# Performance work log

Hardware: AMD Instinct MI355X
Metric: run time of the kernel (lower is better)

Reference implementation:

```python
import jax, jax.numpy as jnp
import numpy as np

N, E = 100000, 1600000
IN, H, C, OUT = 128, 4, 32, 64  # in_channels, heads, hidden_channels, out_channels


def setup_inputs() -> dict:
    key = jax.random.key(0)
    ks = jax.random.split(key, 9)
    x = jax.random.normal(ks[0], (N, IN), dtype=jnp.float32)
    edge_index = jax.random.randint(ks[1], (2, E), 0, N, dtype=jnp.int64)
    s = 1.0 / np.sqrt(IN)
    W = jax.random.uniform(ks[2], (IN, H * C), jnp.float32, -s, s)
    att_src = jax.random.uniform(ks[3], (H, C), jnp.float32, -s, s)
    att_dst = jax.random.uniform(ks[4], (H, C), jnp.float32, -s, s)
    bias = jnp.zeros((H * C,), jnp.float32)
    sl = 1.0 / np.sqrt(H * C)
    lin_w = jax.random.uniform(ks[5], (H * C, OUT), jnp.float32, -sl, sl)
    lin_b = jax.random.uniform(ks[6], (OUT,), jnp.float32, -sl, sl)
    return {"x": x, "edge_index": edge_index, "W": W, "att_src": att_src,
            "att_dst": att_dst, "bias": bias, "lin_w": lin_w, "lin_b": lin_b}


def reference(x, edge_index, W, att_src, att_dst, bias, lin_w, lin_b):
    n = x.shape[0]
    # PyG GATConv default: add self-loops
    loops = jnp.arange(n, dtype=edge_index.dtype)
    src = jnp.concatenate([edge_index[0], loops])  # message sources
    dst = jnp.concatenate([edge_index[1], loops])  # message targets
    h = (x @ W).reshape(n, H, C)                   # [N,H,C]
    a_src = (h * att_src).sum(-1)                  # [N,H]
    a_dst = (h * att_dst).sum(-1)                  # [N,H]
    e = jax.nn.leaky_relu(a_src[src] + a_dst[dst], 0.2)  # [E',H]
    # segment softmax over incoming edges per destination node
    m = jax.ops.segment_max(e, dst, num_segments=n)
    m = jnp.where(jnp.isfinite(m), m, 0.0)
    ex = jnp.exp(e - m[dst])
    denom = jax.ops.segment_sum(ex, dst, num_segments=n)
    alpha = ex / (denom[dst] + 1e-16)              # [E',H]
    agg = jax.ops.segment_sum(h[src] * alpha[:, :, None], dst, num_segments=n)  # [N,H,C]
    out = agg.reshape(n, H * C) + bias
    out = jax.nn.relu(out)  # dropout is identity in eval mode
    return out @ lin_w + lin_b
```

## Files before the change

### kernel.cpp

```cpp
#include <hip/hip_runtime.h>
#include <math.h>

#define NND 100000
#define NED 1600000

#define CAP 64

#define NRANGE 8
#define RNG_NODES ((NND + NRANGE - 1) / NRANGE)
#define NCHUNK 640
#define CHUNK_E (NED / NCHUNK)

#define GEMM_NB (NND / 32)
#define GROUPS 640
#define GRID_NB (GROUPS * 13)

#define OFF_HB    ((size_t)0)
#define OFF_YS    ((size_t)25600000)
#define OFF_ASRC  ((size_t)51200000)
#define OFF_ADST  ((size_t)52800000)
#define OFF_SRT   ((size_t)54400000)
#define OFF_WF    ((size_t)80000000)
#define OFF_CUR   ((size_t)80049152)

typedef __attribute__((ext_vector_type(8))) short short8;
typedef __attribute__((ext_vector_type(4))) float f32x4;

__device__ __forceinline__ float leaky02(float v) { return v > 0.f ? v : 0.2f * v; }

__device__ __forceinline__ unsigned short f2bf(float f) {
    unsigned u = __float_as_uint(f);
    return (unsigned short)((u + 0x7fffu + ((u >> 16) & 1u)) >> 16);
}

__global__ __launch_bounds__(256)
void k_wprep(const float* __restrict__ W, const float* __restrict__ lin_w,
             unsigned short* __restrict__ wf, int* __restrict__ cur) {
    const int idx = blockIdx.x * 256 + threadIdx.x;
    if (blockIdx.x >= 12) {
        const int i = (blockIdx.x - 12) * 256 + threadIdx.x;
        if (i < NND) cur[i] = 0;
        return;
    }
    if (idx < 2048) {
        const int l  = idx & 63;
        const int ks = (idx >> 6) & 3;
        const int ct = (idx >> 8) & 1;
        const int wv = idx >> 9;
        const int col = wv * 32 + ct * 16 + (l & 15);
        const int k0  = ks * 32 + (l >> 4) * 8;
#pragma unroll
        for (int j = 0; j < 8; ++j)
            wf[idx * 8 + j] = f2bf(W[(size_t)(k0 + j) * 128 + col]);
    } else if (idx < 3072) {
        const int i2 = idx - 2048;
        const int l  = i2 & 63;
        const int ks = (i2 >> 6) & 3;
        const int wv = i2 >> 8;
        const int col = wv * 16 + (l & 15);
        const int k0  = ks * 32 + (l >> 4) * 8;
#pragma unroll
        for (int j = 0; j < 8; ++j)
            wf[idx * 8 + j] = f2bf(lin_w[(size_t)(k0 + j) * 64 + col]);
    }
}

__global__ __launch_bounds__(256)
void k_front(const int* __restrict__ esrc, const int* __restrict__ edst,
             int* __restrict__ cur, int* __restrict__ ssrt,
             const float* __restrict__ x, const unsigned short* __restrict__ wf,
             const float* __restrict__ att_s, const float* __restrict__ att_d,
             unsigned short* __restrict__ hb,
             float* __restrict__ a_src, float* __restrict__ a_dst)
{
    __shared__ unsigned short xb[32 * 128];

    const int g = blockIdx.x / 13;
    const int r13 = blockIdx.x % 13;

    if (r13 < 8) {
        const int dlo = r13 * RNG_NODES;
        const int dhi = min(NND, dlo + RNG_NODES);
        const int elo = g * CHUNK_E;
        const int ehi = elo + CHUNK_E;

        int e = elo + threadIdx.x;
        for (; e + 768 < ehi; e += 1024) {
            const int d0 = edst[e];
            const int d1 = edst[e + 256];
            const int d2 = edst[e + 512];
            const int d3 = edst[e + 768];
            const int s0 = esrc[e];
            const int s1 = esrc[e + 256];
            const int s2 = esrc[e + 512];
            const int s3 = esrc[e + 768];
            if (d0 >= dlo && d0 < dhi) { const int p = atomicAdd(&cur[d0], 1); if (p < CAP - 1) ssrt[d0 * CAP + 1 + p] = s0; }
            if (d1 >= dlo && d1 < dhi) { const int p = atomicAdd(&cur[d1], 1); if (p < CAP - 1) ssrt[d1 * CAP + 1 + p] = s1; }
            if (d2 >= dlo && d2 < dhi) { const int p = atomicAdd(&cur[d2], 1); if (p < CAP - 1) ssrt[d2 * CAP + 1 + p] = s2; }
            if (d3 >= dlo && d3 < dhi) { const int p = atomicAdd(&cur[d3], 1); if (p < CAP - 1) ssrt[d3 * CAP + 1 + p] = s3; }
        }
        for (; e < ehi; e += 256) {
            const int d = edst[e];
            if (d >= dlo && d < dhi) {
                const int p = atomicAdd(&cur[d], 1);
                if (p < CAP - 1) ssrt[d * CAP + 1 + p] = esrc[e];
            }
        }
        return;
    }

    const int gb = g * 5 + (r13 - 8);
    if (gb >= GEMM_NB) return;
    const int tid = threadIdx.x;
    const int wv = tid >> 6;
    const int l = tid & 63;
    const int lg = l >> 4;
    const int lc = l & 15;
    const int row0 = gb * 32;

    const float4* x4 = (const float4*)(x + (size_t)row0 * 128);
#pragma unroll
    for (int i = 0; i < 4; ++i) {
        const int g2 = tid + 256 * i;
        const int row = g2 >> 5;
        const int kq = g2 & 31;
        const float4 v = x4[g2];
        uint2 p;
        p.x = (unsigned)f2bf(v.x) | ((unsigned)f2bf(v.y) << 16);
        p.y = (unsigned)f2bf(v.z) | ((unsigned)f2bf(v.w) << 16);
        const int byteoff = (row * 256 + kq * 8) ^ ((row & 7) << 4);
        *(uint2*)((char*)xb + byteoff) = p;
    }

    short8 bf[2][4];
#pragma unroll
    for (int ct = 0; ct < 2; ++ct)
#pragma unroll
        for (int ks = 0; ks < 4; ++ks)
            bf[ct][ks] = *(const short8*)(wf + (size_t)((((wv * 2 + ct) * 4 + ks) * 64 + l) * 8));

    __syncthreads();

    f32x4 acc[2][2];
#pragma unroll
    for (int rt = 0; rt < 2; ++rt)
#pragma unroll
        for (int ct = 0; ct < 2; ++ct)
            acc[rt][ct] = (f32x4){0.f, 0.f, 0.f, 0.f};

#pragma unroll
    for (int ks = 0; ks < 4; ++ks) {
        short8 a[2];
#pragma unroll
        for (int rt = 0; rt < 2; ++rt) {
            const int row = rt * 16 + lc;
            const int byteoff = (row * 256 + (ks * 32 + lg * 8) * 2) ^ ((row & 7) << 4);
            a[rt] = *(const short8*)((const char*)xb + byteoff);
        }
#pragma unroll
        for (int rt = 0; rt < 2; ++rt)
#pragma unroll
            for (int ct = 0; ct < 2; ++ct)
                acc[rt][ct] = __builtin_amdgcn_mfma_f32_16x16x32_bf16(
                    a[rt], bf[ct][ks], acc[rt][ct], 0, 0, 0);
    }

    const int c0 = wv * 32 + lc;
    const float as0 = att_s[c0], as1 = att_s[c0 + 16];
    const float ad0 = att_d[c0], ad1 = att_d[c0 + 16];

#pragma unroll
    for (int rt = 0; rt < 2; ++rt) {
#pragma unroll
        for (int r = 0; r < 4; ++r) {
            const int row = row0 + rt * 16 + lg * 4 + r;
            const float h0 = acc[rt][0][r];
            const float h1 = acc[rt][1][r];
            hb[(size_t)row * 128 + c0]      = f2bf(h0);
            hb[(size_t)row * 128 + c0 + 16] = f2bf(h1);
            float vs = h0 * as0 + h1 * as1;
            float vd = h0 * ad0 + h1 * ad1;
#pragma unroll
            for (int o = 8; o > 0; o >>= 1) {
                vs += __shfl_xor(vs, o, 64);
                vd += __shfl_xor(vd, o, 64);
            }
            if (lc == 0) {
                a_src[row * 4 + wv] = vs;
                a_dst[row * 4 + wv] = vd;
            }
        }
    }
}

__global__ __launch_bounds__(256)
void k_fused(const int* __restrict__ cur, const int* __restrict__ ssrt,
             const float* __restrict__ a_src, const float* __restrict__ a_dst,
             const unsigned short* __restrict__ hb, const float* __restrict__ bias,
             unsigned short* __restrict__ ysb)
{
    __shared__ int   s_src[4][64];
    __shared__ float s_alp[4][64][4];
    const int lane = threadIdx.x & 63;
    const int wv = threadIdx.x >> 6;
    const int d = blockIdx.x * 4 + wv;
    if (d >= NND) return;
    const int cnt = min(cur[d], CAP - 1) + 1;
    const float4 ad = *(const float4*)(a_dst + (size_t)d * 4);

    int s = d;
    float4 ex = make_float4(0.f, 0.f, 0.f, 0.f);
    if (lane < cnt) {
        s = (lane == 0) ? d : ssrt[d * CAP + lane];
        const float4 as = *(const float4*)(a_src + (size_t)s * 4);
        ex.x = __expf(leaky02(as.x + ad.x));
        ex.y = __expf(leaky02(as.y + ad.y));
        ex.z = __expf(leaky02(as.z + ad.z));
        ex.w = __expf(leaky02(as.w + ad.w));
    }
    float4 sm = ex;
#pragma unroll
    for (int o = 32; o > 0; o >>= 1) {
        sm.x += __shfl_xor(sm.x, o, 64);
        sm.y += __shfl_xor(sm.y, o, 64);
        sm.z += __shfl_xor(sm.z, o, 64);
        sm.w += __shfl_xor(sm.w, o, 64);
    }
    const float4 iv = make_float4(1.f / (sm.x + 1e-16f), 1.f / (sm.y + 1e-16f),
                                  1.f / (sm.z + 1e-16f), 1.f / (sm.w + 1e-16f));
    if (lane < cnt) {
        s_src[wv][lane] = s;
        const float4 al = make_float4(ex.x * iv.x, ex.y * iv.y,
                                      ex.z * iv.z, ex.w * iv.w);
        *(float4*)&s_alp[wv][lane][0] = al;
    }

    const int hsel = lane >> 4;
    float accx = 0.f, accy = 0.f;
    int k = 0;
    for (; k + 8 <= cnt; k += 8) {
        int sv[8];
        float Av[8];
        unsigned uv[8];
#pragma unroll
        for (int q = 0; q < 8; ++q) {
            sv[q] = __builtin_amdgcn_readfirstlane(s_src[wv][k + q]);
            Av[q] = s_alp[wv][k + q][hsel];
        }
#pragma unroll
        for (int q = 0; q < 8; ++q)
            uv[q] = *(const unsigned*)(hb + (size_t)sv[q] * 128 + 2 * lane);
#pragma unroll
        for (int q = 0; q < 8; ++q) {
            accx += __uint_as_float(uv[q] << 16) * Av[q];
            accy += __uint_as_float(uv[q] & 0xffff0000u) * Av[q];
        }
    }
    for (; k < cnt; ++k) {
        const int s2 = __builtin_amdgcn_readfirstlane(s_src[wv][k]);
        const float A = s_alp[wv][k][hsel];
        const unsigned u = *(const unsigned*)(hb + (size_t)s2 * 128 + 2 * lane);
        accx += __uint_as_float(u << 16) * A;
        accy += __uint_as_float(u & 0xffff0000u) * A;
    }
    const float2 bb = *(const float2*)(bias + 2 * lane);
    float ox = accx + bb.x, oy = accy + bb.y;
    ox = ox > 0.f ? ox : 0.f;
    oy = oy > 0.f ? oy : 0.f;
    const unsigned up = (unsigned)f2bf(ox) | ((unsigned)f2bf(oy) << 16);
    *(unsigned*)(ysb + (size_t)d * 128 + 2 * lane) = up;
}

__global__ __launch_bounds__(256)
void k_out(const unsigned short* __restrict__ ysb, const unsigned short* __restrict__ wf,
           const float* __restrict__ lin_b, float* __restrict__ out)
{
    __shared__ unsigned short yb[32 * 128];
    const int tid = threadIdx.x;
    const int wv = tid >> 6;
    const int l = tid & 63;
    const int lg = l >> 4;
    const int lc = l & 15;
    const int row0 = blockIdx.x * 32;

    const uint2* ysrc = (const uint2*)(ysb + (size_t)row0 * 128);
#pragma unroll
    for (int i = 0; i < 4; ++i) {
        const int g = tid + 256 * i;
        const int row = g >> 5;
        const int kq = g & 31;
        const uint2 v = ysrc[g];
        const int byteoff = (row * 256 + kq * 8) ^ ((row & 7) << 4);
        *(uint2*)((char*)yb + byteoff) = v;
    }

    short8 bf[4];
#pragma unroll
    for (int ks = 0; ks < 4; ++ks)
        bf[ks] = *(const short8*)(wf + (size_t)((2048 + (wv * 4 + ks) * 64 + l) * 8));

    __syncthreads();

    f32x4 acc[2];
    acc[0] = (f32x4){0.f, 0.f, 0.f, 0.f};
    acc[1] = (f32x4){0.f, 0.f, 0.f, 0.f};

#pragma unroll
    for (int ks = 0; ks < 4; ++ks) {
        short8 a[2];
#pragma unroll
        for (int rt = 0; rt < 2; ++rt) {
            const int row = rt * 16 + lc;
            const int byteoff = (row * 256 + (ks * 32 + lg * 8) * 2) ^ ((row & 7) << 4);
            a[rt] = *(const short8*)((const char*)yb + byteoff);
        }
#pragma unroll
        for (int rt = 0; rt < 2; ++rt)
            acc[rt] = __builtin_amdgcn_mfma_f32_16x16x32_bf16(a[rt], bf[ks], acc[rt], 0, 0, 0);
    }

    const int col = wv * 16 + lc;
    const float lb = lin_b[col];
#pragma unroll
    for (int rt = 0; rt < 2; ++rt) {
#pragma unroll
        for (int r = 0; r < 4; ++r) {
            const int row = row0 + rt * 16 + lg * 4 + r;
            out[(size_t)row * 64 + col] = acc[rt][r] + lb;
        }
    }
}

extern "C" void kernel_launch(void* const* d_in, const int* in_sizes, int n_in,
                              void* d_out, int out_size, void* d_ws, size_t ws_size,
                              hipStream_t stream)
{
    const float* x     = (const float*)d_in[0];
    const int*   ei    = (const int*)  d_in[1];
    const float* W     = (const float*)d_in[2];
    const float* att_s = (const float*)d_in[3];
    const float* att_d = (const float*)d_in[4];
    const float* bias  = (const float*)d_in[5];
    const float* lin_w = (const float*)d_in[6];
    const float* lin_b = (const float*)d_in[7];
    float* out = (float*)d_out;

    const int* esrc = ei;
    const int* edst = ei + NED;

    char* ws = (char*)d_ws;
    unsigned short* hb  = (unsigned short*)(ws + OFF_HB);
    unsigned short* ysb = (unsigned short*)(ws + OFF_YS);
    float* a_src = (float*)(ws + OFF_ASRC);
    float* a_dst = (float*)(ws + OFF_ADST);
    int*   ssrt  = (int*)  (ws + OFF_SRT);
    unsigned short* wf = (unsigned short*)(ws + OFF_WF);
    int*   cur  = (int*)  (ws + OFF_CUR);

    k_wprep<<<12 + (NND + 255) / 256, 256, 0, stream>>>(W, lin_w, wf, cur);

    k_front<<<GRID_NB, 256, 0, stream>>>(esrc, edst, cur, ssrt,
                                         x, wf, att_s, att_d,
                                         hb, a_src, a_dst);

    k_fused<<<(NND + 3) / 4, 256, 0, stream>>>(cur, ssrt, a_src, a_dst,
                                               hb, bias, ysb);

    k_out<<<NND / 32, 256, 0, stream>>>(ysb, wf, lin_b, out);
}
```

Baseline: 172.2 us.

## Fuse attention aggregation with output linear into a single back kernel

Merges the per-destination softmax/aggregation kernel and the output projection MFMA kernel into one kernel. Each block handles 32 destination rows, with each wave processing 8 rows serially, writing the bf16 activations straight into swizzled shared memory and then running the MFMA projection. This removes the global ysb round-trip (write plus reread, about 25 MB) and one kernel launch. In exchange, each wave now covers 8 rows in sequence, so there are fewer independent waves in flight to hide gather latency.

```diff
diff --git a/kernel.cpp b/kernel.cpp
--- a/kernel.cpp
+++ b/kernel.cpp
@@ -16,12 +16,11 @@
 #define GRID_NB (GROUPS * 13)
 
 #define OFF_HB    ((size_t)0)
-#define OFF_YS    ((size_t)25600000)
-#define OFF_ASRC  ((size_t)51200000)
-#define OFF_ADST  ((size_t)52800000)
-#define OFF_SRT   ((size_t)54400000)
-#define OFF_WF    ((size_t)80000000)
-#define OFF_CUR   ((size_t)80049152)
+#define OFF_ASRC  ((size_t)25600000)
+#define OFF_ADST  ((size_t)27200000)
+#define OFF_SRT   ((size_t)28800000)
+#define OFF_WF    ((size_t)54400000)
+#define OFF_CUR   ((size_t)54449152)
 
 typedef __attribute__((ext_vector_type(8))) short short8;
 typedef __attribute__((ext_vector_type(4))) float f32x4;
@@ -194,112 +193,101 @@
 }
 
 __global__ __launch_bounds__(256)
-void k_fused(const int* __restrict__ cur, const int* __restrict__ ssrt,
-             const float* __restrict__ a_src, const float* __restrict__ a_dst,
-             const unsigned short* __restrict__ hb, const float* __restrict__ bias,
-             unsigned short* __restrict__ ysb)
+void k_back(const int* __restrict__ cur, const int* __restrict__ ssrt,
+            const float* __restrict__ a_src, const float* __restrict__ a_dst,
+            const unsigned short* __restrict__ hb, const float* __restrict__ bias,
+            const unsigned short* __restrict__ wf, const float* __restrict__ lin_b,
+            float* __restrict__ out)
 {
+    __shared__ unsigned short yb[32 * 128];
     __shared__ int   s_src[4][64];
     __shared__ float s_alp[4][64][4];
-    const int lane = threadIdx.x & 63;
-    const int wv = threadIdx.x >> 6;
-    const int d = blockIdx.x * 4 + wv;
-    if (d >= NND) return;
-    const int cnt = min(cur[d], CAP - 1) + 1;
-    const float4 ad = *(const float4*)(a_dst + (size_t)d * 4);
-
-    int s = d;
-    float4 ex = make_float4(0.f, 0.f, 0.f, 0.f);
-    if (lane < cnt) {
-        s = (lane == 0) ? d : ssrt[d * CAP + lane];
-        const float4 as = *(const float4*)(a_src + (size_t)s * 4);
-        ex.x = __expf(leaky02(as.x + ad.x));
-        ex.y = __expf(leaky02(as.y + ad.y));
-        ex.z = __expf(leaky02(as.z + ad.z));
-        ex.w = __expf(leaky02(as.w + ad.w));
-    }
-    float4 sm = ex;
-#pragma unroll
-    for (int o = 32; o > 0; o >>= 1) {
-        sm.x += __shfl_xor(sm.x, o, 64);
-        sm.y += __shfl_xor(sm.y, o, 64);
-        sm.z += __shfl_xor(sm.z, o, 64);
-        sm.w += __shfl_xor(sm.w, o, 64);
-    }
-    const float4 iv = make_float4(1.f / (sm.x + 1e-16f), 1.f / (sm.y + 1e-16f),
-                                  1.f / (sm.z + 1e-16f), 1.f / (sm.w + 1e-16f));
-    if (lane < cnt) {
-        s_src[wv][lane] = s;
-        const float4 al = make_float4(ex.x * iv.x, ex.y * iv.y,
-                                      ex.z * iv.z, ex.w * iv.w);
-        *(float4*)&s_alp[wv][lane][0] = al;
-    }
-
+    const int tid = threadIdx.x;
+    const int lane = tid & 63;
+    const int wv = tid >> 6;
+    const int base = blockIdx.x * 32;
+
+    const float2 bb = *(const float2*)(bias + 2 * lane);
     const int hsel = lane >> 4;
-    float accx = 0.f, accy = 0.f;
-    int k = 0;
-    for (; k + 8 <= cnt; k += 8) {
-        int sv[8];
-        float Av[8];
-        unsigned uv[8];
-#pragma unroll
-        for (int q = 0; q < 8; ++q) {
-            sv[q] = __builtin_amdgcn_readfirstlane(s_src[wv][k + q]);
-            Av[q] = s_alp[wv][k + q][hsel];
-        }
-#pragma unroll
-        for (int q = 0; q < 8; ++q)
-            uv[q] = *(const unsigned*)(hb + (size_t)sv[q] * 128 + 2 * lane);
-#pragma unroll
-        for (int q = 0; q < 8; ++q) {
-            accx += __uint_as_float(uv[q] << 16) * Av[q];
-            accy += __uint_as_float(uv[q] & 0xffff0000u) * Av[q];
-        }
-    }
-    for (; k < cnt; ++k) {
-        const int s2 = __builtin_amdgcn_readfirstlane(s_src[wv][k]);
-        const float A = s_alp[wv][k][hsel];
-        const unsigned u = *(const unsigned*)(hb + (size_t)s2 * 128 + 2 * lane);
-        accx += __uint_as_float(u << 16) * A;
-        accy += __uint_as_float(u & 0xffff0000u) * A;
-    }
-    const float2 bb = *(const float2*)(bias + 2 * lane);
-    float ox = accx + bb.x, oy = accy + bb.y;
-    ox = ox > 0.f ? ox : 0.f;
-    oy = oy > 0.f ? oy : 0.f;
-    const unsigned up = (unsigned)f2bf(ox) | ((unsigned)f2bf(oy) << 16);
-    *(unsigned*)(ysb + (size_t)d * 128 + 2 * lane) = up;
-}
-
-__global__ __launch_bounds__(256)
-void k_out(const unsigned short* __restrict__ ysb, const unsigned short* __restrict__ wf,
-           const float* __restrict__ lin_b, float* __restrict__ out)
-{
-    __shared__ unsigned short yb[32 * 128];
-    const int tid = threadIdx.x;
-    const int wv = tid >> 6;
-    const int l = tid & 63;
+#pragma unroll 1
+    for (int i = 0; i < 8; ++i) {
+        const int rloc = wv * 8 + i;
+        const int d = base + rloc;
+        const int cnt = min(cur[d], CAP - 1) + 1;
+        const float4 ad = *(const float4*)(a_dst + (size_t)d * 4);
+
+        int s = d;
+        float4 ex = make_float4(0.f, 0.f, 0.f, 0.f);
+        if (lane < cnt) {
+            s = (lane == 0) ? d : ssrt[d * CAP + lane];
+            const float4 as = *(const float4*)(a_src + (size_t)s * 4);
+            ex.x = __expf(leaky02(as.x + ad.x));
+            ex.y = __expf(leaky02(as.y + ad.y));
+            ex.z = __expf(leaky02(as.z + ad.z));
+            ex.w = __expf(leaky02(as.w + ad.w));
+        }
+        float4 sm = ex;
+#pragma unroll
+        for (int o = 32; o > 0; o >>= 1) {
+            sm.x += __shfl_xor(sm.x, o, 64);
+            sm.y += __shfl_xor(sm.y, o, 64);
+            sm.z += __shfl_xor(sm.z, o, 64);
+            sm.w += __shfl_xor(sm.w, o, 64);
+        }
+        const float4 iv = make_float4(1.f / (sm.x + 1e-16f), 1.f / (sm.y + 1e-16f),
+                                      1.f / (sm.z + 1e-16f), 1.f / (sm.w + 1e-16f));
+        if (lane < cnt) {
+            s_src[wv][lane] = s;
+            const float4 al = make_float4(ex.x * iv.x, ex.y * iv.y,
+                                          ex.z * iv.z, ex.w * iv.w);
+            *(float4*)&s_alp[wv][lane][0] = al;
+        }
+
+        float accx = 0.f, accy = 0.f;
+        int k = 0;
+        for (; k + 8 <= cnt; k += 8) {
+            int sv[8];
+            float Av[8];
+            unsigned uv[8];
+#pragma unroll
+            for (int q = 0; q < 8; ++q) {
+                sv[q] = __builtin_amdgcn_readfirstlane(s_src[wv][k + q]);
+                Av[q] = s_alp[wv][k + q][hsel];
+            }
+#pragma unroll
+            for (int q = 0; q < 8; ++q)
+                uv[q] = *(const unsigned*)(hb + (size_t)sv[q] * 128 + 2 * lane);
+#pragma unroll
+            for (int q = 0; q < 8; ++q) {
+                accx += __uint_as_float(uv[q] << 16) * Av[q];
+                accy += __uint_as_float(uv[q] & 0xffff0000u) * Av[q];
+            }
+        }
+        for (; k < cnt; ++k) {
+            const int s2 = __builtin_amdgcn_readfirstlane(s_src[wv][k]);
+            const float A = s_alp[wv][k][hsel];
+            const unsigned u = *(const unsigned*)(hb + (size_t)s2 * 128 + 2 * lane);
+            accx += __uint_as_float(u << 16) * A;
+            accy += __uint_as_float(u & 0xffff0000u) * A;
+        }
+        float ox = accx + bb.x, oy = accy + bb.y;
+        ox = ox > 0.f ? ox : 0.f;
+        oy = oy > 0.f ? oy : 0.f;
+        const unsigned up = (unsigned)f2bf(ox) | ((unsigned)f2bf(oy) << 16);
+        const int byteoff = (rloc * 256 + lane * 4) ^ ((rloc & 7) << 4);
+        *(unsigned*)((char*)yb + byteoff) = up;
+    }
+
+    __syncthreads();
+
+    const int l = lane;
     const int lg = l >> 4;
     const int lc = l & 15;
-    const int row0 = blockIdx.x * 32;
-
-    const uint2* ysrc = (const uint2*)(ysb + (size_t)row0 * 128);
-#pragma unroll
-    for (int i = 0; i < 4; ++i) {
-        const int g = tid + 256 * i;
-        const int row = g >> 5;
-        const int kq = g & 31;
-        const uint2 v = ysrc[g];
-        const int byteoff = (row * 256 + kq * 8) ^ ((row & 7) << 4);
-        *(uint2*)((char*)yb + byteoff) = v;
-    }
 
     short8 bf[4];
 #pragma unroll
     for (int ks = 0; ks < 4; ++ks)
         bf[ks] = *(const short8*)(wf + (size_t)((2048 + (wv * 4 + ks) * 64 + l) * 8));
-
-    __syncthreads();
 
     f32x4 acc[2];
     acc[0] = (f32x4){0.f, 0.f, 0.f, 0.f};
@@ -325,7 +313,7 @@
     for (int rt = 0; rt < 2; ++rt) {
 #pragma unroll
         for (int r = 0; r < 4; ++r) {
-            const int row = row0 + rt * 16 + lg * 4 + r;
+            const int row = base + rt * 16 + lg * 4 + r;
             out[(size_t)row * 64 + col] = acc[rt][r] + lb;
         }
     }
@@ -350,7 +338,6 @@
 
     char* ws = (char*)d_ws;
     unsigned short* hb  = (unsigned short*)(ws + OFF_HB);
-    unsigned short* ysb = (unsigned short*)(ws + OFF_YS);
     float* a_src = (float*)(ws + OFF_ASRC);
     float* a_dst = (float*)(ws + OFF_ADST);
     int*   ssrt  = (int*)  (ws + OFF_SRT);
@@ -363,8 +350,6 @@
                                          x, wf, att_s, att_d,
                                          hb, a_src, a_dst);
 
-    k_fused<<<(NND + 3) / 4, 256, 0, stream>>>(cur, ssrt, a_src, a_dst,
-                                               hb, bias, ysb);
-
-    k_out<<<NND / 32, 256, 0, stream>>>(ysb, wf, lin_b, out);
-}
+    k_back<<<NND / 32, 256, 0, stream>>>(cur, ssrt, a_src, a_dst,
+                                         hb, bias, wf, lin_b, out);
+}
```

Measured after the change: 174.0 us. No clear change (+1.0%).
